# Kernel tuning notes

Hardware: AMD Instinct MI355X
Metric: run time of the kernel (lower is better)

## Reference

```python
import jax, jax.numpy as jnp
import numpy as np

B, Q, D, H, HD, LP, M = 16, 1, 2048, 16, 128, 2048, 8192
EPS = 1e-5

def _ln(x, w, b):
    mu = jnp.mean(x, axis=-1, keepdims=True)
    var = jnp.mean((x - mu) ** 2, axis=-1, keepdims=True)
    return (x - mu) * jax.lax.rsqrt(var + EPS) * w + b

def setup_inputs() -> dict:
    key = jax.random.key(0)
    ks = jax.random.split(key, 8)
    std = 0.02
    return {
        "input": jax.random.normal(ks[0], (B, Q, D), jnp.float32),
        "past_key": jax.random.normal(ks[1], (B, LP, H, HD), jnp.float32),
        "past_value": jax.random.normal(ks[2], (B, LP, H, HD), jnp.float32),
        "ln0_w": jnp.ones((D,), jnp.float32),
        "ln0_b": jnp.zeros((D,), jnp.float32),
        "ln1_w": jnp.ones((D,), jnp.float32),
        "ln1_b": jnp.zeros((D,), jnp.float32),
        "wqkv": jax.random.normal(ks[3], (3 * D, D), jnp.float32) * std,
        "wo": jax.random.normal(ks[4], (D, D), jnp.float32) * std,
        "fc0_w": jax.random.normal(ks[5], (M, D), jnp.float32) * std,
        "fc0_b": jnp.zeros((M,), jnp.float32),
        "fc1_w": jax.random.normal(ks[6], (D, M), jnp.float32) * std,
        "fc1_b": jnp.zeros((D,), jnp.float32),
    }

def reference(input, past_key, past_value, ln0_w, ln0_b, ln1_w, ln1_b,
              wqkv, wo, fc0_w, fc0_b, fc1_w, fc1_b):
    # norm0 + fused QKV projection (no bias)
    x = _ln(input, ln0_w, ln0_b)                       # [B,Q,D]
    qkv = (x @ wqkv.T).reshape(B, Q, 3, H, HD)
    q, k, v = qkv[:, :, 0], qkv[:, :, 1], qkv[:, :, 2]  # each [B,Q,H,HD]
    # append to KV cache
    k = jnp.concatenate([past_key, k], axis=1)          # [B,LP+Q,H,HD]
    v = jnp.concatenate([past_value, v], axis=1)
    # decode attention; q_len == 1 so no causal mask is applied (matches source)
    scores = jnp.einsum('nqhd,nkhd->nhqk', q, k) / (HD ** 0.5)
    attn = jax.nn.softmax(scores.astype(jnp.float32), axis=-1).astype(scores.dtype)
    attn_out = jnp.einsum('nhql,nlhd->nqhd', attn, v).reshape(B, Q, D)
    attn_out = attn_out @ wo.T
    h = input + attn_out
    # MLP2 with exact (erf) GELU as in torch F.gelu
    y = _ln(h, ln1_w, ln1_b)
    y = jax.nn.gelu(y @ fc0_w.T + fc0_b, approximate=False) @ fc1_w.T + fc1_b
    return h + y
```

## Files before the change

### kernel.cpp

```cpp
#include <hip/hip_runtime.h>
#include <math.h>

typedef __attribute__((ext_vector_type(4))) float f32x4;
typedef __attribute__((ext_vector_type(4))) _Float16 f16x4;

#define B_  16
#define D_  2048
#define H_  16
#define HD_ 128
#define LP_ 2048
#define M_  8192
#define QKV_R (3 * D_)
#define SCALE 0.08838834764831845f
#define NSPLIT 32
#define KPS 64

__device__ inline float wave_sum(float v) {
  for (int m = 32; m > 0; m >>= 1) v += __shfl_xor(v, m);
  return v;
}

__global__ void ln_kernel(const float* __restrict__ x, const float* __restrict__ w,
                          const float* __restrict__ bb, float* __restrict__ o) {
  __shared__ float sred[4];
  int b = blockIdx.x, t = threadIdx.x;
  const float* xr = x + (size_t)b * D_;
  f32x4 v0 = *(const f32x4*)(xr + t * 8);
  f32x4 v1 = *(const f32x4*)(xr + t * 8 + 4);
  float s = (v0[0] + v0[1] + v0[2] + v0[3]) + (v1[0] + v1[1] + v1[2] + v1[3]);
  s = wave_sum(s);
  if ((t & 63) == 0) sred[t >> 6] = s;
  __syncthreads();
  float mu = (sred[0] + sred[1] + sred[2] + sred[3]) * (1.0f / D_);
  __syncthreads();
  float sq = 0.f;
  for (int i = 0; i < 4; i++) {
    float d0 = v0[i] - mu; sq += d0 * d0;
    float d1 = v1[i] - mu; sq += d1 * d1;
  }
  sq = wave_sum(sq);
  if ((t & 63) == 0) sred[t >> 6] = sq;
  __syncthreads();
  float var = (sred[0] + sred[1] + sred[2] + sred[3]) * (1.0f / D_);
  float rs = rsqrtf(var + 1e-5f);
  f32x4 w0 = *(const f32x4*)(w + t * 8), w1 = *(const f32x4*)(w + t * 8 + 4);
  f32x4 c0 = *(const f32x4*)(bb + t * 8), c1 = *(const f32x4*)(bb + t * 8 + 4);
  f32x4 o0, o1;
  for (int i = 0; i < 4; i++) {
    o0[i] = (v0[i] - mu) * rs * w0[i] + c0[i];
    o1[i] = (v1[i] - mu) * rs * w1[i] + c1[i];
  }
  *(f32x4*)(o + (size_t)b * D_ + t * 8) = o0;
  *(f32x4*)(o + (size_t)b * D_ + t * 8 + 4) = o1;
}

__global__ void gemv_k(const float* __restrict__ W, const float* __restrict__ X,
                       float* __restrict__ part, int R, int K, int kc) {
  int wave = threadIdx.x >> 6, lane = threadIdx.x & 63;
  int j0 = (blockIdx.x * 4 + wave) * 16;
  int k0 = blockIdx.y * kc;
  int col = lane & 15;
  int kg  = (lane >> 4) << 2;
  const float* wp = W + (size_t)(j0 + col) * K + k0 + kg;
  const float* xp = X + (size_t)col * K + k0 + kg;
  f32x4 acc = {0.f, 0.f, 0.f, 0.f};
  #pragma unroll 4
  for (int kk = 0; kk < kc; kk += 16) {
    f32x4 av = *(const f32x4*)xp; xp += 16;
    f32x4 bv = *(const f32x4*)wp; wp += 16;
    f16x4 ah, bh;
    for (int i = 0; i < 4; i++) { ah[i] = (_Float16)av[i]; bh[i] = (_Float16)bv[i]; }
    acc = __builtin_amdgcn_mfma_f32_16x16x16f16(ah, bh, acc, 0, 0, 0);
  }
  *(f32x4*)(part + ((size_t)blockIdx.y * R + j0 + col) * 16 + kg) = acc;
}

__global__ void reduce_plain(const float* __restrict__ part, float* __restrict__ out,
                             int R, int S) {
  int i = blockIdx.x * 256 + threadIdx.x;
  int j = i >> 4, b = i & 15;
  float s = 0.f;
  for (int k = 0; k < S; k++) s += part[(size_t)k * R * 16 + i];
  out[(size_t)b * R + j] = s;
}
__global__ void reduce_resid(const float* __restrict__ part, const float* __restrict__ resid,
                             float* __restrict__ out, int R, int S) {
  int i = blockIdx.x * 256 + threadIdx.x;
  int j = i >> 4, b = i & 15;
  float s = 0.f;
  for (int k = 0; k < S; k++) s += part[(size_t)k * R * 16 + i];
  out[(size_t)b * R + j] = resid[(size_t)b * R + j] + s;
}
__global__ void reduce_bias_gelu(const float* __restrict__ part, const float* __restrict__ bias,
                                 float* __restrict__ out, int R, int S) {
  int i = blockIdx.x * 256 + threadIdx.x;
  int j = i >> 4, b = i & 15;
  float s = 0.f;
  for (int k = 0; k < S; k++) s += part[(size_t)k * R * 16 + i];
  float u = s + bias[j];
  out[(size_t)b * R + j] = 0.5f * u * (1.0f + erff(u * 0.70710678118654752f));
}
__global__ void reduce_bias_resid(const float* __restrict__ part, const float* __restrict__ bias,
                                  const float* __restrict__ resid, float* __restrict__ out,
                                  int R, int S) {
  int i = blockIdx.x * 256 + threadIdx.x;
  int j = i >> 4, b = i & 15;
  float s = 0.f;
  for (int k = 0; k < S; k++) s += part[(size_t)k * R * 16 + i];
  out[(size_t)b * R + j] = resid[(size_t)b * R + j] + s + bias[j];
}

__global__ void attn_part(const float* __restrict__ qkv, const float* __restrict__ pk,
                          const float* __restrict__ pv, float* __restrict__ pml,
                          float* __restrict__ pacc) {
  int b = blockIdx.x, split = blockIdx.y;
  int t = threadIdx.x;
  int h = t >> 4, d0 = (t & 15) * 8;
  __shared__ float s_s[16][KPS + 1];

  f32x4 q0 = *(const f32x4*)(qkv + (size_t)b * QKV_R + h * HD_ + d0);
  f32x4 q1 = *(const f32x4*)(qkv + (size_t)b * QKV_R + h * HD_ + d0 + 4);
  for (int i = 0; i < 4; i++) { q0[i] *= SCALE; q1[i] *= SCALE; }

  const float* kb = pk + ((size_t)b * LP_ + split * KPS) * D_ + t * 8;
  #pragma unroll 4
  for (int l = 0; l < KPS; l++) {
    f32x4 k0 = *(const f32x4*)(kb + (size_t)l * D_);
    f32x4 k1 = *(const f32x4*)(kb + (size_t)l * D_ + 4);
    float d = q0[0]*k0[0] + q0[1]*k0[1] + q0[2]*k0[2] + q0[3]*k0[3]
            + q1[0]*k1[0] + q1[1]*k1[1] + q1[2]*k1[2] + q1[3]*k1[3];
    d += __shfl_xor(d, 1); d += __shfl_xor(d, 2);
    d += __shfl_xor(d, 4); d += __shfl_xor(d, 8);
    if ((t & 15) == 0) s_s[h][l] = d;
  }
  __syncthreads();

  int l0 = (t & 15) * 4;
  float sv0 = s_s[h][l0], sv1 = s_s[h][l0 + 1], sv2 = s_s[h][l0 + 2], sv3 = s_s[h][l0 + 3];
  float m = fmaxf(fmaxf(sv0, sv1), fmaxf(sv2, sv3));
  m = fmaxf(m, __shfl_xor(m, 1)); m = fmaxf(m, __shfl_xor(m, 2));
  m = fmaxf(m, __shfl_xor(m, 4)); m = fmaxf(m, __shfl_xor(m, 8));
  sv0 = __expf(sv0 - m); sv1 = __expf(sv1 - m);
  sv2 = __expf(sv2 - m); sv3 = __expf(sv3 - m);
  float L = sv0 + sv1 + sv2 + sv3;
  L += __shfl_xor(L, 1); L += __shfl_xor(L, 2);
  L += __shfl_xor(L, 4); L += __shfl_xor(L, 8);
  s_s[h][l0] = sv0; s_s[h][l0 + 1] = sv1; s_s[h][l0 + 2] = sv2; s_s[h][l0 + 3] = sv3;
  if ((t & 15) == 0) {
    pml[((b * NSPLIT + split) * H_ + h) * 2]     = m;
    pml[((b * NSPLIT + split) * H_ + h) * 2 + 1] = L;
  }
  __syncthreads();

  const float* vb = pv + ((size_t)b * LP_ + split * KPS) * D_ + t * 8;
  f32x4 a0 = {0.f, 0.f, 0.f, 0.f}, a1 = {0.f, 0.f, 0.f, 0.f};
  #pragma unroll 4
  for (int l = 0; l < KPS; l++) {
    f32x4 v0 = *(const f32x4*)(vb + (size_t)l * D_);
    f32x4 v1 = *(const f32x4*)(vb + (size_t)l * D_ + 4);
    float p = s_s[h][l];
    for (int i = 0; i < 4; i++) { a0[i] += p * v0[i]; a1[i] += p * v1[i]; }
  }
  size_t oi = (((size_t)b * NSPLIT + split) * H_ + h) * HD_ + d0;
  *(f32x4*)(pacc + oi) = a0;
  *(f32x4*)(pacc + oi + 4) = a1;
}

__global__ void attn_comb(const float* __restrict__ qkv, const float* __restrict__ pml,
                          const float* __restrict__ pacc, float* __restrict__ attn_out) {
  int bh = blockIdx.x, b = bh >> 4, hh = bh & 15;
  int t = threadIdx.x;
  __shared__ float sred[2];
  float qv = qkv[(size_t)b * QKV_R + hh * HD_ + t];
  float kn = qkv[(size_t)b * QKV_R + D_ + hh * HD_ + t];
  float d = qv * kn;
  d = wave_sum(d);
  if ((t & 63) == 0) sred[t >> 6] = d;
  __syncthreads();
  float s_new = (sred[0] + sred[1]) * SCALE;
  float vn = qkv[(size_t)b * QKV_R + 2 * D_ + hh * HD_ + t];
  float M = s_new;
  for (int s = 0; s < NSPLIT; s++)
    M = fmaxf(M, pml[((b * NSPLIT + s) * H_ + hh) * 2]);
  float en = __expf(s_new - M);
  float L = en;
  float o = en * vn;
  for (int s = 0; s < NSPLIT; s++) {
    float ms = pml[((b * NSPLIT + s) * H_ + hh) * 2];
    float ls = pml[((b * NSPLIT + s) * H_ + hh) * 2 + 1];
    float e = __expf(ms - M);
    L += ls * e;
    o += pacc[(((size_t)b * NSPLIT + s) * H_ + hh) * HD_ + t] * e;
  }
  attn_out[(size_t)b * D_ + hh * HD_ + t] = o / L;
}

extern "C" void kernel_launch(void* const* d_in, const int* in_sizes, int n_in,
                              void* d_out, int out_size, void* d_ws, size_t ws_size,
                              hipStream_t stream) {
  const float* input  = (const float*)d_in[0];
  const float* pk     = (const float*)d_in[1];
  const float* pv     = (const float*)d_in[2];
  const float* ln0_w  = (const float*)d_in[3];
  const float* ln0_b  = (const float*)d_in[4];
  const float* ln1_w  = (const float*)d_in[5];
  const float* ln1_b  = (const float*)d_in[6];
  const float* wqkv   = (const float*)d_in[7];
  const float* wo     = (const float*)d_in[8];
  const float* fc0_w  = (const float*)d_in[9];
  const float* fc0_b  = (const float*)d_in[10];
  const float* fc1_w  = (const float*)d_in[11];
  const float* fc1_b  = (const float*)d_in[12];
  float* out = (float*)d_out;

  char* wsb = (char*)d_ws;
  float* x_ln     = (float*)(wsb + 0);
  float* qkv      = (float*)(wsb + 131072);
  float* attn_out = (float*)(wsb + 524288);
  float* hbuf     = (float*)(wsb + 655360);
  float* y0       = (float*)(wsb + 786432);
  float* act      = (float*)(wsb + 917504);
  float* pml      = (float*)(wsb + 1441792);
  float* pacc     = (float*)(wsb + 1507328);
  float* part     = (float*)(wsb + 5701632);

  ln_kernel<<<16, 256, 0, stream>>>(input, ln0_w, ln0_b, x_ln);
  gemv_k<<<dim3(96, 8), 256, 0, stream>>>(wqkv, x_ln, part, QKV_R, D_, 256);
  reduce_plain<<<384, 256, 0, stream>>>(part, qkv, QKV_R, 8);
  attn_part<<<dim3(B_, NSPLIT), 256, 0, stream>>>(qkv, pk, pv, pml, pacc);
  attn_comb<<<256, 128, 0, stream>>>(qkv, pml, pacc, attn_out);
  gemv_k<<<dim3(32, 16), 256, 0, stream>>>(wo, attn_out, part, D_, D_, 128);
  reduce_resid<<<128, 256, 0, stream>>>(part, input, hbuf, D_, 16);
  ln_kernel<<<16, 256, 0, stream>>>(hbuf, ln1_w, ln1_b, y0);
  gemv_k<<<dim3(128, 4), 256, 0, stream>>>(fc0_w, y0, part, M_, D_, 512);
  reduce_bias_gelu<<<512, 256, 0, stream>>>(part, fc0_b, act, M_, 4);
  gemv_k<<<dim3(32, 16), 256, 0, stream>>>(fc1_w, act, part, D_, M_, 512);
  reduce_bias_resid<<<128, 256, 0, stream>>>(part, fc1_b, hbuf, out, D_, 16);
}
```

Baseline: 197.4 us.

## Fuse attention split into single-pass online softmax with more splits

Rewrites the split-KV attention kernel to load K and V rows together and compute an online (running max) softmax in registers. This removes the shared-memory score buffer, the two barriers and the separate V pass. Splits double from 32 to 64 with 32 keys each for more blocks and memory parallelism, and exponentials switch to exp2 with log2e folded into the scale. The cost is extra rescale multiplies per key, more partial results for the combine kernel to read, and relocated workspace buffers.

```diff
diff --git a/kernel.cpp b/kernel.cpp
--- a/kernel.cpp
+++ b/kernel.cpp
@@ -12,8 +12,9 @@
 #define M_  8192
 #define QKV_R (3 * D_)
 #define SCALE 0.08838834764831845f
-#define NSPLIT 32
-#define KPS 64
+#define LOG2E 1.4426950408889634f
+#define NSPLIT 64
+#define KPS 32
 
 __device__ inline float wave_sum(float v) {
   for (int m = 32; m > 0; m >>= 1) v += __shfl_xor(v, m);
@@ -115,53 +116,51 @@
                           float* __restrict__ pacc) {
   int b = blockIdx.x, split = blockIdx.y;
   int t = threadIdx.x;
-  int h = t >> 4, d0 = (t & 15) * 8;
-  __shared__ float s_s[16][KPS + 1];
-
-  f32x4 q0 = *(const f32x4*)(qkv + (size_t)b * QKV_R + h * HD_ + d0);
-  f32x4 q1 = *(const f32x4*)(qkv + (size_t)b * QKV_R + h * HD_ + d0 + 4);
-  for (int i = 0; i < 4; i++) { q0[i] *= SCALE; q1[i] *= SCALE; }
-
-  const float* kb = pk + ((size_t)b * LP_ + split * KPS) * D_ + t * 8;
-  #pragma unroll 4
-  for (int l = 0; l < KPS; l++) {
-    f32x4 k0 = *(const f32x4*)(kb + (size_t)l * D_);
-    f32x4 k1 = *(const f32x4*)(kb + (size_t)l * D_ + 4);
-    float d = q0[0]*k0[0] + q0[1]*k0[1] + q0[2]*k0[2] + q0[3]*k0[3]
-            + q1[0]*k1[0] + q1[1]*k1[1] + q1[2]*k1[2] + q1[3]*k1[3];
-    d += __shfl_xor(d, 1); d += __shfl_xor(d, 2);
-    d += __shfl_xor(d, 4); d += __shfl_xor(d, 8);
-    if ((t & 15) == 0) s_s[h][l] = d;
-  }
-  __syncthreads();
-
-  int l0 = (t & 15) * 4;
-  float sv0 = s_s[h][l0], sv1 = s_s[h][l0 + 1], sv2 = s_s[h][l0 + 2], sv3 = s_s[h][l0 + 3];
-  float m = fmaxf(fmaxf(sv0, sv1), fmaxf(sv2, sv3));
-  m = fmaxf(m, __shfl_xor(m, 1)); m = fmaxf(m, __shfl_xor(m, 2));
-  m = fmaxf(m, __shfl_xor(m, 4)); m = fmaxf(m, __shfl_xor(m, 8));
-  sv0 = __expf(sv0 - m); sv1 = __expf(sv1 - m);
-  sv2 = __expf(sv2 - m); sv3 = __expf(sv3 - m);
-  float L = sv0 + sv1 + sv2 + sv3;
-  L += __shfl_xor(L, 1); L += __shfl_xor(L, 2);
-  L += __shfl_xor(L, 4); L += __shfl_xor(L, 8);
-  s_s[h][l0] = sv0; s_s[h][l0 + 1] = sv1; s_s[h][l0 + 2] = sv2; s_s[h][l0 + 3] = sv3;
+  int h = t >> 4;
+  size_t rowbase = ((size_t)b * LP_ + (size_t)split * KPS) * D_ + t * 8;
+  const float* kb = pk + rowbase;
+  const float* vb = pv + rowbase;
+  f32x4 q0 = *(const f32x4*)(qkv + (size_t)b * QKV_R + t * 8);
+  f32x4 q1 = *(const f32x4*)(qkv + (size_t)b * QKV_R + t * 8 + 4);
+  const float s2 = SCALE * LOG2E;
+  for (int i = 0; i < 4; i++) { q0[i] *= s2; q1[i] *= s2; }
+
+  f32x4 a0 = {0.f, 0.f, 0.f, 0.f}, a1 = {0.f, 0.f, 0.f, 0.f};
+  float m2 = -1e30f, den = 0.f;
+
+  for (int l0 = 0; l0 < KPS; l0 += 4) {
+    f32x4 k0[4], k1[4], v0[4], v1[4];
+    #pragma unroll
+    for (int c = 0; c < 4; c++) {
+      size_t off = (size_t)(l0 + c) * D_;
+      k0[c] = *(const f32x4*)(kb + off);
+      k1[c] = *(const f32x4*)(kb + off + 4);
+      v0[c] = *(const f32x4*)(vb + off);
+      v1[c] = *(const f32x4*)(vb + off + 4);
+    }
+    #pragma unroll
+    for (int c = 0; c < 4; c++) {
+      float s = q0[0]*k0[c][0] + q0[1]*k0[c][1] + q0[2]*k0[c][2] + q0[3]*k0[c][3]
+              + q1[0]*k1[c][0] + q1[1]*k1[c][1] + q1[2]*k1[c][2] + q1[3]*k1[c][3];
+      s += __shfl_xor(s, 1); s += __shfl_xor(s, 2);
+      s += __shfl_xor(s, 4); s += __shfl_xor(s, 8);
+      float mn = fmaxf(m2, s);
+      float corr = exp2f(m2 - mn);
+      float p = exp2f(s - mn);
+      m2 = mn;
+      den = den * corr + p;
+      for (int i = 0; i < 4; i++) {
+        a0[i] = a0[i] * corr + p * v0[c][i];
+        a1[i] = a1[i] * corr + p * v1[c][i];
+      }
+    }
+  }
+
   if ((t & 15) == 0) {
-    pml[((b * NSPLIT + split) * H_ + h) * 2]     = m;
-    pml[((b * NSPLIT + split) * H_ + h) * 2 + 1] = L;
-  }
-  __syncthreads();
-
-  const float* vb = pv + ((size_t)b * LP_ + split * KPS) * D_ + t * 8;
-  f32x4 a0 = {0.f, 0.f, 0.f, 0.f}, a1 = {0.f, 0.f, 0.f, 0.f};
-  #pragma unroll 4
-  for (int l = 0; l < KPS; l++) {
-    f32x4 v0 = *(const f32x4*)(vb + (size_t)l * D_);
-    f32x4 v1 = *(const f32x4*)(vb + (size_t)l * D_ + 4);
-    float p = s_s[h][l];
-    for (int i = 0; i < 4; i++) { a0[i] += p * v0[i]; a1[i] += p * v1[i]; }
-  }
-  size_t oi = (((size_t)b * NSPLIT + split) * H_ + h) * HD_ + d0;
+    pml[((b * NSPLIT + split) * H_ + h) * 2]     = m2;
+    pml[((b * NSPLIT + split) * H_ + h) * 2 + 1] = den;
+  }
+  size_t oi = (((size_t)b * NSPLIT + split) * H_ + h) * HD_ + (t & 15) * 8;
   *(f32x4*)(pacc + oi) = a0;
   *(f32x4*)(pacc + oi + 4) = a1;
 }
@@ -177,18 +176,18 @@
   d = wave_sum(d);
   if ((t & 63) == 0) sred[t >> 6] = d;
   __syncthreads();
-  float s_new = (sred[0] + sred[1]) * SCALE;
+  float s_new = (sred[0] + sred[1]) * SCALE * LOG2E;
   float vn = qkv[(size_t)b * QKV_R + 2 * D_ + hh * HD_ + t];
   float M = s_new;
   for (int s = 0; s < NSPLIT; s++)
     M = fmaxf(M, pml[((b * NSPLIT + s) * H_ + hh) * 2]);
-  float en = __expf(s_new - M);
+  float en = exp2f(s_new - M);
   float L = en;
   float o = en * vn;
   for (int s = 0; s < NSPLIT; s++) {
     float ms = pml[((b * NSPLIT + s) * H_ + hh) * 2];
     float ls = pml[((b * NSPLIT + s) * H_ + hh) * 2 + 1];
-    float e = __expf(ms - M);
+    float e = exp2f(ms - M);
     L += ls * e;
     o += pacc[(((size_t)b * NSPLIT + s) * H_ + hh) * HD_ + t] * e;
   }
@@ -221,8 +220,8 @@
   float* y0       = (float*)(wsb + 786432);
   float* act      = (float*)(wsb + 917504);
   float* pml      = (float*)(wsb + 1441792);
-  float* pacc     = (float*)(wsb + 1507328);
-  float* part     = (float*)(wsb + 5701632);
+  float* pacc     = (float*)(wsb + 1572864);
+  float* part     = (float*)(wsb + 9961472);
 
   ln_kernel<<<16, 256, 0, stream>>>(input, ln0_w, ln0_b, x_ln);
   gemv_k<<<dim3(96, 8), 256, 0, stream>>>(wqkv, x_ln, part, QKV_R, D_, 256);
```

After: 209.7 us. 6.2% more time.
